# Performance work log

Hardware: AMD Instinct MI355X
Metric: run time of the kernel (lower is better)

The kernel has to match this reference:

```python
import jax, jax.numpy as jnp
import numpy as np

N = 200000
IN_CH = 128
HIDDEN = [512, 512, 256]
NUM_TYPES = 10


def hetero_linear(x, types, W, b):
    # y[n] = x[n] @ W[types[n]] + b[types[n]]
    # Loop over the small fixed set of types (grouped GEMM as masked dense GEMMs).
    out = jnp.zeros((x.shape[0], W.shape[2]), dtype=x.dtype)
    for t in range(W.shape[0]):
        yt = x @ W[t] + b[t]
        out = out + jnp.where((types == t)[:, None], yt, jnp.zeros((), x.dtype))
    return out


def setup_inputs() -> dict:
    key = jax.random.key(0)
    ks = jax.random.split(key, 8)
    dims = [IN_CH] + HIDDEN
    inp = {
        "x": jax.random.normal(ks[0], (N, IN_CH), dtype=jnp.float32),
        "atom_types": jax.random.randint(ks[1], (N,), 0, NUM_TYPES, dtype=jnp.int32),
    }
    for i in range(3):
        fan_in = dims[i]
        scale = 1.0 / np.sqrt(fan_in)
        inp[f"W{i}"] = jax.random.normal(ks[2 + 2 * i], (NUM_TYPES, dims[i], dims[i + 1]), dtype=jnp.float32) * scale
        inp[f"b{i}"] = jax.random.normal(ks[3 + 2 * i], (NUM_TYPES, dims[i + 1]), dtype=jnp.float32) * scale
    return inp


def reference(x, atom_types, W0, b0, W1, b1, W2, b2):
    h = jax.nn.relu(hetero_linear(x, atom_types, W0, b0))
    h = jax.nn.relu(hetero_linear(h, atom_types, W1, b1))
    return hetero_linear(h, atom_types, W2, b2)
```

## Files before the change

kernel.cpp:

```cpp
#include <hip/hip_runtime.h>
#include <stdint.h>

typedef float  f32x4  __attribute__((ext_vector_type(4)));
typedef short  bf16x8 __attribute__((ext_vector_type(8)));

#define TYPES 10
#define D_IN  128
#define D_H1  512
#define D_H2  512
#define D_OUT 256

__device__ __forceinline__ unsigned short f2bf(float f) {
  union { float f; unsigned u; } v; v.f = f;
  unsigned u = v.u;
  return (unsigned short)((u + 0x7FFFu + ((u >> 16) & 1u)) >> 16);
}

__device__ __forceinline__ void async16(void* lds, const void* g) {
  __builtin_amdgcn_global_load_lds(
      (const __attribute__((address_space(1))) void*)g,
      (__attribute__((address_space(3))) void*)lds, 16, 0, 0);
}

__global__ void k_init(int* meta) {
  if (threadIdx.x < 48) meta[threadIdx.x] = 0;
}

__global__ void k_hist(const int* __restrict__ types, int n, int* __restrict__ meta) {
  __shared__ int lc[TYPES];
  if (threadIdx.x < TYPES) lc[threadIdx.x] = 0;
  __syncthreads();
  int i = blockIdx.x * 256 + threadIdx.x;
  if (i < n) atomicAdd(&lc[types[i]], 1);
  __syncthreads();
  if (threadIdx.x < TYPES && lc[threadIdx.x]) atomicAdd(&meta[threadIdx.x], lc[threadIdx.x]);
}

__global__ void k_scan(int* meta) {
  if (threadIdx.x == 0) {
    int off = 0;
    for (int t = 0; t < TYPES; ++t) {
      meta[16 + t] = off;
      off += ((meta[t] + 255) >> 8) << 8;
    }
    meta[26] = off;
  }
}

__global__ void k_scatter(const int* __restrict__ types, int n,
                          int* __restrict__ meta, int* __restrict__ perm) {
  __shared__ int lc[TYPES], lbase[TYPES];
  if (threadIdx.x < TYPES) lc[threadIdx.x] = 0;
  __syncthreads();
  int i = blockIdx.x * 256 + threadIdx.x;
  int t = 0, loc = 0;
  bool ok = i < n;
  if (ok) { t = types[i]; loc = atomicAdd(&lc[t], 1); }
  __syncthreads();
  if (threadIdx.x < TYPES) {
    int c = lc[threadIdx.x];
    lbase[threadIdx.x] = c ? atomicAdd(&meta[32 + threadIdx.x], c) : 0;
  }
  __syncthreads();
  if (ok) perm[meta[16 + t] + lbase[t] + loc] = i;
}

__global__ void k_gather(const float* __restrict__ x, const int* __restrict__ perm,
                         const int* __restrict__ meta, unsigned short* __restrict__ xs) {
  int p = blockIdx.x * 8 + (threadIdx.x >> 5);
  if (p >= meta[26]) return;
  int t = 0;
  while (p >= meta[17 + t]) t++;
  int e = (threadIdx.x & 31) * 4;
  unsigned short o0, o1, o2, o3;
  if (p - meta[16 + t] < meta[t]) {
    const float4 v = *(const float4*)(x + (size_t)perm[p] * D_IN + e);
    o0 = f2bf(v.x); o1 = f2bf(v.y); o2 = f2bf(v.z); o3 = f2bf(v.w);
  } else {
    o0 = o1 = o2 = o3 = 0;
  }
  *(ushort4*)(xs + (size_t)p * D_IN + e) = make_ushort4(o0, o1, o2, o3);
}

__global__ void k_wtrans_all(const float* __restrict__ W0a, const float* __restrict__ W1a,
                             const float* __restrict__ W2a,
                             unsigned short* __restrict__ wt0, unsigned short* __restrict__ wt1,
                             unsigned short* __restrict__ wt2) {
  int b = blockIdx.x;
  const float* W; unsigned short* Wt; int K, NOUT, t, local;
  if (b < 160)      { W = W0a; Wt = wt0; K = 128; NOUT = 512; t = b / 16; local = b % 16; }
  else if (b < 800) { b -= 160; W = W1a; Wt = wt1; K = 512; NOUT = 512; t = b / 64; local = b % 64; }
  else              { b -= 800; W = W2a; Wt = wt2; K = 512; NOUT = 256; t = b / 32; local = b % 32; }
  int ntn = NOUT >> 6;
  int kb = local / ntn, nb = local % ntn;
  __shared__ unsigned short tile[64][65];
  const float* src = W + (size_t)t * K * NOUT + (size_t)(kb * 64) * NOUT + nb * 64;
  int c = threadIdx.x & 63;
  int r0 = threadIdx.x >> 6;
  #pragma unroll
  for (int i = 0; i < 16; ++i) {
    int r = r0 * 16 + i;
    tile[r][c] = f2bf(src[(size_t)r * NOUT + c]);
  }
  __syncthreads();
  unsigned short* dst = Wt + (size_t)t * NOUT * K + (size_t)(nb * 64) * K + kb * 64;
  #pragma unroll
  for (int i = 0; i < 16; ++i) {
    int nn = r0 * 16 + i;
    dst[(size_t)nn * K + c] = tile[c][nn];
  }
}

template <int K, int NOUT, bool RELU, bool FINAL>
__launch_bounds__(512, 2)
__global__ void k_gemm(const unsigned short* __restrict__ A,
                       const unsigned short* __restrict__ Wt,
                       const float* __restrict__ bias,
                       unsigned short* __restrict__ H,
                       float* __restrict__ OUT,
                       const int* __restrict__ meta,
                       const int* __restrict__ perm) {
  constexpr int nKT = K / 64;
  __shared__ char lds[131072];

  int NXB = gridDim.x;
  int nwg = NXB * (int)gridDim.y;
  int raw = blockIdx.x + blockIdx.y * NXB;
  int q = nwg >> 3, rr = nwg & 7;
  int xcd = raw & 7, idx = raw >> 3;
  int swz = (xcd < rr ? xcd * (q + 1) : rr * (q + 1) + (xcd - rr) * q) + idx;
  int bx = swz % NXB, by = swz / NXB;

  int row0 = by * 256;
  if (row0 >= meta[26]) return;
  int t = 0;
  while (row0 >= meta[17 + t]) t++;
  int seg = meta[16 + t], cnt = meta[t];
  int tid = threadIdx.x, lane = tid & 63, wid = tid >> 6;
  int wr = (wid >> 2) * 128, wc = (wid & 3) * 64;
  int col0 = bx * 256;
  const char* Ag = (const char*)(A + (size_t)row0 * K);
  const char* Bg = (const char*)(Wt + ((size_t)t * NOUT + col0) * K);

  int gsrc = ((tid & 7) ^ ((tid >> 3) & 7)) * 16;
  const char* aS = Ag + (size_t)(tid >> 3) * (2 * K) + gsrc;
  const char* bS = Bg + (size_t)(((tid >> 3) & 31) + ((tid >> 3) >> 5) * 64) * (2 * K) + gsrc;

  auto stage = [&](int kt, int sub) {
    if (kt >= nKT) return;
    int h = sub & 1, du = kt & 1;
    char* dst = lds + ((sub < 2) ? 0 : 65536) + (du * 2 + h) * 16384 + wid * 1024;
    const char* src = (sub < 2 ? aS + (size_t)(h * 64) * (2 * K)
                               : bS + (size_t)(h * 32) * (2 * K)) + (size_t)kt * 128;
    async16(dst,        src);
    async16(dst + 8192, src + (size_t)128 * (2 * K));
  };

  f32x4 acc[8][4] = {};
  int rA = lane & 15, qoff = (lane >> 4) * 16, xr = (lane & 7) << 4;
  int lrA = (wid >> 2) * 64;
  int clB = (wid & 3) * 32;

  stage(0, 0); stage(0, 1); stage(0, 2); stage(0, 3); stage(1, 0);
  asm volatile("s_waitcnt vmcnt(4)" ::: "memory");
  __builtin_amdgcn_s_barrier();

  for (int g = 0; g < nKT; ++g) {
    int d = g & 1;
    const char* Ad = lds + d * 32768;
    const char* Bd = lds + 65536 + d * 32768;
    bf16x8 a[4][2], b0[2][2], b1[2][2];
    #pragma unroll
    for (int rel = 0; rel < 4; ++rel) {
      __builtin_amdgcn_sched_barrier(0);
      constexpr int MH[4] = {0, 0, 1, 1};
      constexpr int NH[4] = {0, 1, 1, 0};
      const int mh = MH[rel], nh = NH[rel];
      if (rel == 0 || rel == 2) {
        const char* Au = Ad + mh * 16384;
        #pragma unroll
        for (int m = 0; m < 4; ++m) {
          int lr = lrA + m * 16 + rA;
          #pragma unroll
          for (int kk = 0; kk < 2; ++kk)
            a[m][kk] = *(const bf16x8*)(Au + ((lr * 128 + kk * 64 + qoff) ^ xr));
        }
      }
      if (rel == 0) {
        const char* Bu = Bd;
        #pragma unroll
        for (int nn = 0; nn < 2; ++nn) {
          int cl = clB + nn * 16 + rA;
          #pragma unroll
          for (int kk = 0; kk < 2; ++kk)
            b0[nn][kk] = *(const bf16x8*)(Bu + ((cl * 128 + kk * 64 + qoff) ^ xr));
        }
      }
      if (rel == 1) {
        const char* Bu = Bd + 16384;
        #pragma unroll
        for (int nn = 0; nn < 2; ++nn) {
          int cl = clB + nn * 16 + rA;
          #pragma unroll
          for (int kk = 0; kk < 2; ++kk)
            b1[nn][kk] = *(const bf16x8*)(Bu + ((cl * 128 + kk * 64 + qoff) ^ xr));
        }
      }
      if      (rel == 0) { stage(g + 1, 1); stage(g + 1, 2); }
      else if (rel == 1) stage(g + 1, 3);
      else if (rel == 3) stage(g + 2, 0);
      __builtin_amdgcn_s_barrier();
      asm volatile("s_waitcnt lgkmcnt(0)" ::: "memory");
      __builtin_amdgcn_sched_barrier(0);
      __builtin_amdgcn_s_setprio(1);
      #pragma unroll
      for (int kk = 0; kk < 2; ++kk)
        #pragma unroll
        for (int m = 0; m < 4; ++m)
          #pragma unroll
          for (int nn = 0; nn < 2; ++nn) {
            const bf16x8 bop = nh ? b1[nn][kk] : b0[nn][kk];
            acc[mh * 4 + m][nh * 2 + nn] = __builtin_amdgcn_mfma_f32_16x16x32_bf16(
                a[m][kk], bop, acc[mh * 4 + m][nh * 2 + nn], 0, 0, 0);
          }
      __builtin_amdgcn_s_setprio(0);
      if (rel == 0) {
        if (g + 1 < nKT) asm volatile("s_waitcnt vmcnt(6)" ::: "memory");
        else             asm volatile("s_waitcnt vmcnt(0)" ::: "memory");
      } else if (rel == 3 && g + 1 < nKT) {
        if (g + 2 < nKT) asm volatile("s_waitcnt vmcnt(4)" ::: "memory");
        else             asm volatile("s_waitcnt vmcnt(2)" ::: "memory");
      }
      __builtin_amdgcn_s_barrier();
    }
  }

  int cA = lane & 15, rE = (lane >> 4) * 4;
  float bv[4];
  #pragma unroll
  for (int ni = 0; ni < 4; ++ni) bv[ni] = bias[t * NOUT + col0 + wc + ni * 16 + cA];
  char* cb = (char*)lds;

  if (!FINAL) {
    #pragma unroll
    for (int mi = 0; mi < 8; ++mi)
      #pragma unroll
      for (int e = 0; e < 4; ++e) {
        int row = wr + mi * 16 + rE + e;
        int sw = (row & 7) << 4;
        #pragma unroll
        for (int ni = 0; ni < 4; ++ni) {
          float v = acc[mi][ni][e] + bv[ni];
          if (RELU) v = fmaxf(v, 0.f);
          int col = wc + ni * 16 + cA;
          *(unsigned short*)(cb + ((row * 512 + col * 2) ^ sw)) = f2bf(v);
        }
      }
    __builtin_amdgcn_s_barrier();
    #pragma unroll 4
    for (int r = 0; r < 16; ++r) {
      int row = wid * 32 + r * 2 + (lane >> 5);
      int addr = row * 512 + ((((lane & 31) * 16)) ^ ((row & 7) << 4));
      bf16x8 v = *(const bf16x8*)(cb + addr);
      *(bf16x8*)(H + (size_t)(row0 + row) * NOUT + col0 + (lane & 31) * 8) = v;
    }
  } else {
    int myhalf = (wid & 3) >> 1;
    #pragma unroll
    for (int p = 0; p < 2; ++p) {
      if (myhalf == p) {
        int colh = wc & 127;
        #pragma unroll
        for (int mi = 0; mi < 8; ++mi)
          #pragma unroll
          for (int e = 0; e < 4; ++e) {
            int row = wr + mi * 16 + rE + e;
            int sw = (row & 7) << 4;
            #pragma unroll
            for (int ni = 0; ni < 4; ++ni) {
              float v = acc[mi][ni][e] + bv[ni];
              if (RELU) v = fmaxf(v, 0.f);
              int col = colh + ni * 16 + cA;
              *(float*)(cb + ((row * 512 + col * 4) ^ sw)) = v;
            }
          }
      }
      __builtin_amdgcn_s_barrier();
      #pragma unroll 4
      for (int r = 0; r < 16; ++r) {
        int row = wid * 32 + r * 2 + (lane >> 5);
        int gr = row0 + row;
        int addr = row * 512 + ((((lane & 31) * 16)) ^ ((row & 7) << 4));
        float4 v = *(const float4*)(cb + addr);
        if (gr - seg < cnt) {
          int pr = perm[gr];
          *(float4*)(OUT + (size_t)pr * NOUT + p * (NOUT / 2) + (lane & 31) * 4) = v;
        }
      }
      if (p == 0) __builtin_amdgcn_s_barrier();
    }
  }
}

extern "C" void kernel_launch(void* const* d_in, const int* in_sizes, int n_in,
                              void* d_out, int out_size, void* d_ws, size_t ws_size,
                              hipStream_t stream) {
  const float* x     = (const float*)d_in[0];
  const int*   types = (const int*)d_in[1];
  const float* W0    = (const float*)d_in[2];
  const float* b0    = (const float*)d_in[3];
  const float* W1    = (const float*)d_in[4];
  const float* b1    = (const float*)d_in[5];
  const float* W2    = (const float*)d_in[6];
  const float* b2    = (const float*)d_in[7];
  float* out = (float*)d_out;
  int n = in_sizes[1];
  int RB = (n + 255) / 256 + TYPES;
  size_t NPAD = (size_t)RB * 256;

  char* ws = (char*)d_ws;
  int* meta = (int*)ws;
  int* perm = (int*)(ws + 1024);
  size_t off = 1024 + NPAD * 4;
  off = (off + 255) & ~(size_t)255;
  unsigned short* wt0 = (unsigned short*)(ws + off); off += (size_t)TYPES * D_H1 * D_IN * 2;
  unsigned short* wt1 = (unsigned short*)(ws + off); off += (size_t)TYPES * D_H2 * D_H1 * 2;
  unsigned short* wt2 = (unsigned short*)(ws + off); off += (size_t)TYPES * D_OUT * D_H2 * 2;
  off = (off + 255) & ~(size_t)255;
  unsigned short* B1 = (unsigned short*)(ws + off); off += NPAD * 512 * 2;
  unsigned short* B2 = (unsigned short*)(ws + off); off += NPAD * 512 * 2;

  int hb = (n + 255) / 256;
  k_init<<<1, 64, 0, stream>>>(meta);
  k_hist<<<hb, 256, 0, stream>>>(types, n, meta);
  k_scan<<<1, 64, 0, stream>>>(meta);
  k_scatter<<<hb, 256, 0, stream>>>(types, n, meta, perm);
  k_gather<<<RB * 32, 256, 0, stream>>>(x, perm, meta, B1);
  k_wtrans_all<<<1120, 256, 0, stream>>>(W0, W1, W2, wt0, wt1, wt2);

  k_gemm<D_IN, D_H1, true,  false><<<dim3(D_H1 / 256, RB), 512, 0, stream>>>(B1, wt0, b0, B2, nullptr, meta, perm);
  k_gemm<D_H1, D_H2, true,  false><<<dim3(D_H2 / 256, RB), 512, 0, stream>>>(B2, wt1, b1, B1, nullptr, meta, perm);
  k_gemm<D_H2, D_OUT, false, true ><<<dim3(D_OUT / 256, RB), 512, 0, stream>>>(B1, wt2, b2, nullptr, out, meta, perm);
}
```

Measured before the change: 423.9 us.

## Restructure GEMM main loop from four sub-phases into two larger phases

```diff
diff --git a/kernel.cpp b/kernel.cpp
--- a/kernel.cpp
+++ b/kernel.cpp
@@ -162,7 +162,7 @@
   int clB = (wid & 3) * 32;
 
   stage(0, 0); stage(0, 1); stage(0, 2); stage(0, 3); stage(1, 0);
-  asm volatile("s_waitcnt vmcnt(4)" ::: "memory");
+  asm volatile("s_waitcnt vmcnt(2)" ::: "memory");
   __builtin_amdgcn_s_barrier();
 
   for (int g = 0; g < nKT; ++g) {
@@ -170,69 +170,65 @@
     const char* Ad = lds + d * 32768;
     const char* Bd = lds + 65536 + d * 32768;
     bf16x8 a[4][2], b0[2][2], b1[2][2];
-    #pragma unroll
-    for (int rel = 0; rel < 4; ++rel) {
-      __builtin_amdgcn_sched_barrier(0);
-      constexpr int MH[4] = {0, 0, 1, 1};
-      constexpr int NH[4] = {0, 1, 1, 0};
-      const int mh = MH[rel], nh = NH[rel];
-      if (rel == 0 || rel == 2) {
-        const char* Au = Ad + mh * 16384;
-        #pragma unroll
-        for (int m = 0; m < 4; ++m) {
-          int lr = lrA + m * 16 + rA;
-          #pragma unroll
-          for (int kk = 0; kk < 2; ++kk)
-            a[m][kk] = *(const bf16x8*)(Au + ((lr * 128 + kk * 64 + qoff) ^ xr));
-        }
+
+    #pragma unroll
+    for (int m = 0; m < 4; ++m) {
+      int lr = lrA + m * 16 + rA;
+      #pragma unroll
+      for (int kk = 0; kk < 2; ++kk)
+        a[m][kk] = *(const bf16x8*)(Ad + ((lr * 128 + kk * 64 + qoff) ^ xr));
+    }
+    #pragma unroll
+    for (int nn = 0; nn < 2; ++nn) {
+      int cl = clB + nn * 16 + rA;
+      #pragma unroll
+      for (int kk = 0; kk < 2; ++kk) {
+        b0[nn][kk] = *(const bf16x8*)(Bd +         ((cl * 128 + kk * 64 + qoff) ^ xr));
+        b1[nn][kk] = *(const bf16x8*)(Bd + 16384 + ((cl * 128 + kk * 64 + qoff) ^ xr));
       }
-      if (rel == 0) {
-        const char* Bu = Bd;
+    }
+    stage(g + 1, 1); stage(g + 1, 2); stage(g + 1, 3);
+    __builtin_amdgcn_s_barrier();
+    asm volatile("s_waitcnt lgkmcnt(0)" ::: "memory");
+    __builtin_amdgcn_s_setprio(1);
+    #pragma unroll
+    for (int kk = 0; kk < 2; ++kk)
+      #pragma unroll
+      for (int m = 0; m < 4; ++m)
         #pragma unroll
         for (int nn = 0; nn < 2; ++nn) {
-          int cl = clB + nn * 16 + rA;
-          #pragma unroll
-          for (int kk = 0; kk < 2; ++kk)
-            b0[nn][kk] = *(const bf16x8*)(Bu + ((cl * 128 + kk * 64 + qoff) ^ xr));
+          acc[m][nn]     = __builtin_amdgcn_mfma_f32_16x16x32_bf16(a[m][kk], b0[nn][kk], acc[m][nn],     0, 0, 0);
+          acc[m][2 + nn] = __builtin_amdgcn_mfma_f32_16x16x32_bf16(a[m][kk], b1[nn][kk], acc[m][2 + nn], 0, 0, 0);
         }
-      }
-      if (rel == 1) {
-        const char* Bu = Bd + 16384;
+    __builtin_amdgcn_s_setprio(0);
+    __builtin_amdgcn_s_barrier();
+
+    #pragma unroll
+    for (int m = 0; m < 4; ++m) {
+      int lr = lrA + m * 16 + rA;
+      #pragma unroll
+      for (int kk = 0; kk < 2; ++kk)
+        a[m][kk] = *(const bf16x8*)(Ad + 16384 + ((lr * 128 + kk * 64 + qoff) ^ xr));
+    }
+    stage(g + 2, 0);
+    __builtin_amdgcn_s_barrier();
+    asm volatile("s_waitcnt lgkmcnt(0)" ::: "memory");
+    __builtin_amdgcn_s_setprio(1);
+    #pragma unroll
+    for (int kk = 0; kk < 2; ++kk)
+      #pragma unroll
+      for (int m = 0; m < 4; ++m)
         #pragma unroll
         for (int nn = 0; nn < 2; ++nn) {
-          int cl = clB + nn * 16 + rA;
-          #pragma unroll
-          for (int kk = 0; kk < 2; ++kk)
-            b1[nn][kk] = *(const bf16x8*)(Bu + ((cl * 128 + kk * 64 + qoff) ^ xr));
+          acc[4 + m][2 + nn] = __builtin_amdgcn_mfma_f32_16x16x32_bf16(a[m][kk], b1[nn][kk], acc[4 + m][2 + nn], 0, 0, 0);
+          acc[4 + m][nn]     = __builtin_amdgcn_mfma_f32_16x16x32_bf16(a[m][kk], b0[nn][kk], acc[4 + m][nn],     0, 0, 0);
         }
-      }
-      if      (rel == 0) { stage(g + 1, 1); stage(g + 1, 2); }
-      else if (rel == 1) stage(g + 1, 3);
-      else if (rel == 3) stage(g + 2, 0);
-      __builtin_amdgcn_s_barrier();
-      asm volatile("s_waitcnt lgkmcnt(0)" ::: "memory");
-      __builtin_amdgcn_sched_barrier(0);
-      __builtin_amdgcn_s_setprio(1);
-      #pragma unroll
-      for (int kk = 0; kk < 2; ++kk)
-        #pragma unroll
-        for (int m = 0; m < 4; ++m)
-          #pragma unroll
-          for (int nn = 0; nn < 2; ++nn) {
-            const bf16x8 bop = nh ? b1[nn][kk] : b0[nn][kk];
-            acc[mh * 4 + m][nh * 2 + nn] = __builtin_amdgcn_mfma_f32_16x16x32_bf16(
-                a[m][kk], bop, acc[mh * 4 + m][nh * 2 + nn], 0, 0, 0);
-          }
-      __builtin_amdgcn_s_setprio(0);
-      if (rel == 0) {
-        if (g + 1 < nKT) asm volatile("s_waitcnt vmcnt(6)" ::: "memory");
-        else             asm volatile("s_waitcnt vmcnt(0)" ::: "memory");
-      } else if (rel == 3 && g + 1 < nKT) {
-        if (g + 2 < nKT) asm volatile("s_waitcnt vmcnt(4)" ::: "memory");
-        else             asm volatile("s_waitcnt vmcnt(2)" ::: "memory");
-      }
-      __builtin_amdgcn_s_barrier();
-    }
+    __builtin_amdgcn_s_setprio(0);
+    if (g + 1 < nKT) {
+      if (g + 2 < nKT) asm volatile("s_waitcnt vmcnt(2)" ::: "memory");
+      else             asm volatile("s_waitcnt vmcnt(0)" ::: "memory");
+    }
+    __builtin_amdgcn_s_barrier();
   }
 
   int cA = lane & 15, rE = (lane >> 4) * 4;
```

After: 433.2 us. 1.02x slower.
